# Kernel tuning notes

Measured on AMD Instinct MI355X. Metric: run time of the kernel, lower is better.

Reference implementation:

```python
import jax, jax.numpy as jnp
import numpy as np

EPS = 1e-5  # torch BatchNorm1d default eps


def _bn(x, axes):
    # BatchNorm in training mode with gamma=1, beta=0 (torch init values):
    # normalize with biased batch statistics over the given axes.
    m = x.mean(axes, keepdims=True)
    v = x.var(axes, keepdims=True)
    return (x - m) * jax.lax.rsqrt(v + EPS)


def setup_inputs() -> dict:
    key = jax.random.key(0)
    ks = jax.random.split(key, 12)
    N, M = 50000, 12
    OF, F, E, H = 92, 64, 41, 128
    Z = 2 * F + E  # 169 = concat(node, nbr_node, edge)

    def w(k, shape, fan):
        return jax.random.normal(k, shape, jnp.float32) * np.float32(1.0 / np.sqrt(fan))

    return {
        "node_fea": jax.random.normal(ks[0], (N, OF), jnp.float32),
        "edge_fea": jax.random.uniform(ks[1], (N, M, E), dtype=jnp.float32),
        "nbr_offset": jax.random.randint(ks[2], (N, M, 3), -1, 2).astype(jnp.float32),
        "atom_pos": jax.random.uniform(ks[3], (N, 3), dtype=jnp.float32) * 10.0,
        "cells": jnp.broadcast_to(jnp.eye(3, dtype=jnp.float32) * 10.0, (N, 3, 3))
                 + jax.random.normal(ks[4], (N, 3, 3), jnp.float32) * 0.1,
        "edge_idx": jax.random.randint(ks[5], (N, M), 0, N),
        "W_emb": w(ks[6], (OF, F), OF), "b_emb": jnp.zeros((F,), jnp.float32),
        "W_pre_node": w(ks[7], (3, Z, 2 * F), Z), "b_pre_node": jnp.zeros((3, 2 * F), jnp.float32),
        "W_pre_edge": w(ks[8], (3, Z, 2 * E), Z), "b_pre_edge": jnp.zeros((3, 2 * E), jnp.float32),
        "W_dist": w(ks[9], (Z, H), Z), "b_dist": jnp.zeros((H,), jnp.float32),
        "W_const": w(ks[10], (Z, H), Z), "b_const": jnp.zeros((H,), jnp.float32),
    }


def reference(node_fea, edge_fea, nbr_offset, atom_pos, cells, edge_idx,
              W_emb, b_emb, W_pre_node, b_pre_node, W_pre_edge, b_pre_edge,
              W_dist, b_dist, W_const, b_const):
    N, M = edge_idx.shape
    lrelu = jax.nn.leaky_relu  # torch LeakyReLU default slope 0.01
    sig = jax.nn.sigmoid
    sp = jax.nn.softplus

    # get_distance: neighbor Cartesian positions via unit-cell offsets
    off_cart = jnp.einsum('nmi,nij->nmj', nbr_offset, cells)         # (N,M,3)
    diff = atom_pos[edge_idx] + off_cart - atom_pos[:, None, :]       # (N,M,3)
    distance = jnp.sqrt(jnp.sum(diff * diff, -1, keepdims=True) + 1e-12)  # (N,M,1)

    node = node_fea @ W_emb + b_emb  # embedding -> (N,64)

    for l in range(W_pre_node.shape[0]):  # n_conv = 3 ConvLayers
        nbr = node[edge_idx]  # gather (N,M,F)
        z = jnp.concatenate(
            [jnp.broadcast_to(node[:, None, :], (N, M, node.shape[-1])), nbr, edge_fea],
            axis=2)  # (N,M,169)
        # node branch: linear -> BN -> sigmoid*leakyrelu gate -> sum over M -> BN -> residual
        zn = _bn(z @ W_pre_node[l] + b_pre_node[l], (0, 1))  # (N,M,128)
        nf, nc = jnp.split(zn, 2, axis=2)
        aggr = jnp.sum(sig(nf) * lrelu(nc), axis=1)           # (N,64)
        node = lrelu(node + _bn(aggr, (0,)))
        # edge branch: linear -> BN -> gate -> BN -> residual
        ze = _bn(z @ W_pre_edge[l] + b_pre_edge[l], (0, 1))   # (N,M,82)
        ef, ec = jnp.split(ze, 2, axis=2)
        edge_fea = lrelu(edge_fea + _bn(sig(ef) * lrelu(ec), (0, 1)))

    nbr = node[edge_idx]
    bond_fea = jnp.concatenate(
        [jnp.broadcast_to(node[:, None, :], (N, M, node.shape[-1])), nbr, edge_fea],
        axis=2)  # (N,M,169)

    # n_h_dist == 1 branch: softplus(BN(linear) + distance), mean over channels
    bd = sp(_bn(bond_fea @ W_dist + b_dist, (0, 1)) + distance)
    bd = jnp.mean(bd, axis=2, keepdims=True)                  # (N,M,1)
    # n_h_const == 1 branch: softplus(BN(linear)), mean over channels, / N
    bc = sp(_bn(bond_fea @ W_const + b_const, (0, 1)))
    bc = jnp.mean(bc, axis=2, keepdims=True) / N              # (N,M,1)

    return jnp.concatenate([bd, bc], axis=2)                  # (N,M,2)
```

## Files before the change

kernel.cpp:

```cpp
#include <hip/hip_runtime.h>
#include <math.h>

#define NN 50000
#define MM 12
#define NM 600000
#define OF 92
#define FF 64
#define EE 41
#define ES 48
#define ZZ 169
#define EFO 128
#define ECO 192
#define RPB 96
#define NPB 8
#define NBLK 6250
#define KP 200
#define KSTEPS 6
#define MT 6
#define NSLICE 64
#define PSTRIDE 1024

typedef __bf16 bf16x8 __attribute__((ext_vector_type(8)));
typedef float  f32x4  __attribute__((ext_vector_type(4)));

__device__ __forceinline__ float lrelu(float x){ return fmaxf(x, 0.01f*x); }
__device__ __forceinline__ float sigm(float x){ return __builtin_amdgcn_rcpf(1.f+__expf(-x)); }
__device__ __forceinline__ float softpl(float x){ return fmaxf(x,0.f) + __logf(1.f+__expf(-fabsf(x))); }
__device__ __forceinline__ unsigned short f2bf(float f){
    __bf16 h = (__bf16)f;
    return __builtin_bit_cast(unsigned short, h);
}
__device__ __forceinline__ float b2f(unsigned short u){
    unsigned int b = ((unsigned int)u) << 16;
    return __builtin_bit_cast(float, b);
}
__device__ __forceinline__ unsigned short f2h(float f){
    _Float16 h = (_Float16)f;
    return __builtin_bit_cast(unsigned short, h);
}
__device__ __forceinline__ float h2f(unsigned short u){
    return (float)__builtin_bit_cast(_Float16, u);
}

__global__ __launch_bounds__(256) void pack_w(const float* __restrict__ Wn,
    const float* __restrict__ We, const float* __restrict__ Wd,
    const float* __restrict__ Wc, unsigned short* __restrict__ dst)
{
    int idx = blockIdx.x*256 + threadIdx.x;
    if (idx >= 4*49152) return;
    int j    = idx & 7;
    int lane = (idx >> 3) & 63;
    int ntks = (idx >> 9) % 96;
    int L    = idx / 49152;
    int nt = ntks & 15, ks = ntks >> 4;
    int k   = ks*32 + (lane>>4)*8 + j;
    int col = nt*16 + (lane&15);
    float v = 0.f;
    if (k < ZZ) {
        if (L < 3) {
            if (col < 128)                       v = Wn[((size_t)L*ZZ + k)*128 + col];
            else if (col >= EFO && col < EFO+EE) v = We[((size_t)L*ZZ + k)*82 + (col-EFO)];
            else if (col >= ECO && col < ECO+EE) v = We[((size_t)L*ZZ + k)*82 + 41 + (col-ECO)];
        } else {
            if (col < 128) v = Wd[(size_t)k*128 + col];
            else           v = Wc[(size_t)k*128 + (col-128)];
        }
    }
    dst[idx] = f2bf(v);
}

__global__ __launch_bounds__(256) void k_dist(const float* __restrict__ off,
    const float* __restrict__ apos, const float* __restrict__ cells,
    const int* __restrict__ eidx, float* __restrict__ distb)
{
    int idx = blockIdx.x*256 + threadIdx.x;
    if (idx >= NM) return;
    int n = idx / MM;
    const float* o  = off + (size_t)idx*3;
    const float* cl = cells + (size_t)n*9;
    int n2 = eidx[idx];
    float o0=o[0], o1=o[1], o2=o[2];
    float dd = 1e-12f;
    #pragma unroll
    for (int j=0;j<3;j++){
        float oc = o0*cl[0*3+j] + o1*cl[1*3+j] + o2*cl[2*3+j];
        float d = apos[(size_t)n2*3+j] + oc - apos[(size_t)n*3+j];
        dd += d*d;
    }
    distb[idx] = sqrtf(dd);
}

__global__ __launch_bounds__(256) void k_cvt(const float* __restrict__ src,
    unsigned short* __restrict__ e)
{
    int idx = blockIdx.x*256 + threadIdx.x;
    if (idx >= NM*ES) return;
    int gr = idx / ES;
    int c  = idx - gr*ES;
    e[idx] = (c < EE) ? f2bf(src[(size_t)gr*EE + c]) : (unsigned short)0;
}

__global__ __launch_bounds__(256) void k_emb(const float* __restrict__ nf,
    const float* __restrict__ W, const float* __restrict__ b,
    unsigned short* __restrict__ node0)
{
    int idx = blockIdx.x*256 + threadIdx.x;
    if (idx >= NN*FF) return;
    int n = idx >> 6, c = idx & 63;
    float s = b[c];
    for (int k=0;k<OF;k++) s = fmaf(nf[(size_t)n*OF+k], W[k*FF+c], s);
    node0[idx] = f2bf(s);
}

__global__ __launch_bounds__(256) void k_red(float* __restrict__ P,
    float* __restrict__ dst, int lo, int hi)
{
    for (int c = lo + threadIdx.x; c < hi; c += 256) {
        float s = 0.f;
        #pragma unroll 8
        for (int sl = 0; sl < NSLICE; ++sl) s += P[sl*PSTRIDE + c];
        dst[c] = s;
        #pragma unroll 8
        for (int sl = 0; sl < NSLICE; ++sl) P[sl*PSTRIDE + c] = 0.f;
    }
}

__device__ __forceinline__ void stage_z(unsigned short* __restrict__ Zl,
    const unsigned short* __restrict__ node_src, const unsigned short* __restrict__ edge_src,
    const int* __restrict__ eidx, int n0, int tid)
{
    const int gr0 = n0 * MM;
    #pragma unroll
    for (int it=0; it<3; ++it){
        int i = it*256 + tid;
        int row = i >> 3, ch = i & 7;
        int n = n0 + row/MM;
        uint4 v = *(const uint4*)(node_src + (size_t)n*FF + ch*8);
        *(uint4*)(Zl + row*KP + ch*8) = v;
    }
    #pragma unroll
    for (int it=0; it<3; ++it){
        int i = it*256 + tid;
        int row = i >> 3, ch = i & 7;
        int n2 = eidx[gr0 + row];
        uint4 v = *(const uint4*)(node_src + (size_t)n2*FF + ch*8);
        *(uint4*)(Zl + row*KP + 64 + ch*8) = v;
    }
    #pragma unroll
    for (int it=0; it<3; ++it){
        int i = it*256 + tid;
        int row = i >> 3, ch = i & 7;
        uint4 v = make_uint4(0u,0u,0u,0u);
        if (ch < 6) v = *(const uint4*)(edge_src + (size_t)(gr0+row)*ES + ch*8);
        *(uint4*)(Zl + row*KP + 128 + ch*8) = v;
    }
}

__device__ __forceinline__ void mfma_core(const unsigned short* __restrict__ Zl,
    const unsigned short* __restrict__ Wpk, int w, int lane, f32x4 (&acc)[MT][4])
{
    const int quad = lane >> 4, li = lane & 15;
    #pragma unroll
    for (int mt=0;mt<MT;mt++)
        #pragma unroll
        for (int t=0;t<4;t++) acc[mt][t] = (f32x4){0.f,0.f,0.f,0.f};

    #pragma unroll 2
    for (int ks=0; ks<KSTEPS; ++ks) {
        bf16x8 bfr[4];
        #pragma unroll
        for (int t=0;t<4;t++){
            int nt = w + 4*t;
            bfr[t] = *(const bf16x8*)(Wpk + (((ks*16 + nt)*64 + lane) << 3));
        }
        bf16x8 afr[MT];
        #pragma unroll
        for (int mt=0;mt<MT;mt++){
            int row = mt*16 + li;
            afr[mt] = *(const bf16x8*)(Zl + row*KP + ks*32 + quad*8);
        }
        #pragma unroll
        for (int mt=0;mt<MT;mt++)
            #pragma unroll
            for (int t=0;t<4;t++)
                acc[mt][t] = __builtin_amdgcn_mfma_f32_16x16x32_bf16(afr[mt], bfr[t], acc[mt][t], 0, 0, 0);
    }
}

__device__ __forceinline__ void stats_epi(const f32x4 (&acc)[MT][4], int w, int lane,
    float* __restrict__ Ps)
{
    const int quad = lane>>4, li = lane&15;
    #pragma unroll
    for (int t=0;t<4;t++){
        float s=0.f, q=0.f;
        #pragma unroll
        for (int mt=0;mt<MT;mt++)
            #pragma unroll
            for (int r=0;r<4;r++){ float v = acc[mt][t][r]; s+=v; q = fmaf(v,v,q); }
        s += __shfl_xor(s,16); s += __shfl_xor(s,32);
        q += __shfl_xor(q,16); q += __shfl_xor(q,32);
        if (quad == 0) {
            int col = t*64 + w*16 + li;
            atomicAdd(&Ps[col], s);
            atomicAdd(&Ps[256+col], q);
        }
    }
}

__global__ __launch_bounds__(256) void k_stats(
    const unsigned short* __restrict__ node_src, const unsigned short* __restrict__ edge_src,
    const int* __restrict__ eidx, const unsigned short* __restrict__ Wpk,
    float* __restrict__ Pst)
{
    __shared__ unsigned short Zl[RPB*KP];
    const int tid = threadIdx.x, w = tid>>6, lane = tid&63;
    const int n0 = blockIdx.x * NPB;
    stage_z(Zl, node_src, edge_src, eidx, n0, tid);
    __syncthreads();
    f32x4 acc[MT][4];
    mfma_core(Zl, Wpk, w, lane, acc);
    float* Ps = Pst + (size_t)(blockIdx.x & (NSLICE-1))*PSTRIDE;
    stats_epi(acc, w, lane, Ps);
}

__global__ __launch_bounds__(256) void k_gemm(
    const unsigned short* __restrict__ node_src, const unsigned short* __restrict__ edge_src,
    const int* __restrict__ eidx, const unsigned short* __restrict__ Wpk,
    float* __restrict__ Pst, ushort4* __restrict__ Y)
{
    __shared__ unsigned short Zl[RPB*KP];
    const int tid = threadIdx.x, w = tid>>6, lane = tid&63;
    const int b = blockIdx.x;
    const int n0 = b * NPB;
    stage_z(Zl, node_src, edge_src, eidx, n0, tid);
    __syncthreads();
    f32x4 acc[MT][4];
    mfma_core(Zl, Wpk, w, lane, acc);
    #pragma unroll
    for (int mt=0;mt<MT;mt++)
        #pragma unroll
        for (int t=0;t<4;t++){
            ushort4 h;
            h.x = f2h(acc[mt][t][0]); h.y = f2h(acc[mt][t][1]);
            h.z = f2h(acc[mt][t][2]); h.w = f2h(acc[mt][t][3]);
            Y[((size_t)b*96 + mt*16 + t*4 + w)*64 + lane] = h;
        }
    float* Ps = Pst + (size_t)(blockIdx.x & (NSLICE-1))*PSTRIDE;
    stats_epi(acc, w, lane, Ps);
}

__device__ __forceinline__ void apply_epi(float (&vals)[4], int mt,
    int quad, int cg, bool ce_ok, const float sc[4], const float bi[4],
    int r, int gr0, float* __restrict__ gL, unsigned short* __restrict__ gbuf,
    float& pg, float& pq)
{
    int row = mt*16 + quad*4 + r;
    float nf = fmaf(vals[0], sc[0], bi[0]);
    float nc = fmaf(vals[1], sc[1], bi[1]);
    gL[row*68 + cg] = sigm(nf) * lrelu(nc);
    if (ce_ok) {
        float ef = fmaf(vals[2], sc[2], bi[2]);
        float ec = fmaf(vals[3], sc[3], bi[3]);
        float gv = sigm(ef)*lrelu(ec);
        gbuf[(size_t)(gr0+row)*ES + cg] = f2bf(gv);
        pg += gv; pq = fmaf(gv,gv,pq);
    }
}

__device__ __forceinline__ void apply_tail(float pg, float pq, int tid, int quad,
    int cg, bool ce_ok, int n0, const float* __restrict__ gL,
    float* __restrict__ aggr, float* __restrict__ aS, float* __restrict__ aQ,
    float* __restrict__ gS, float* __restrict__ gQ)
{
    pg += __shfl_xor(pg,16); pg += __shfl_xor(pg,32);
    pq += __shfl_xor(pq,16); pq += __shfl_xor(pq,32);
    if (quad==0 && ce_ok){ atomicAdd(&gS[cg], pg); atomicAdd(&gQ[cg], pq); }
    __syncthreads();
    if (tid < 64) {
        float sAcc=0.f, sQq=0.f;
        #pragma unroll
        for (int nl=0; nl<NPB; nl++){
            float vsum = 0.f;
            #pragma unroll
            for (int jj=0;jj<MM;jj++) vsum += gL[(nl*MM+jj)*68 + tid];
            aggr[(size_t)(n0+nl)*64 + tid] = vsum;
            sAcc += vsum; sQq = fmaf(vsum,vsum,sQq);
        }
        atomicAdd(&aS[tid], sAcc);
        atomicAdd(&aQ[tid], sQq);
    }
}

__global__ __launch_bounds__(256) void k_apply_y(
    const ushort4* __restrict__ Y,
    const float* __restrict__ preS, const float* __restrict__ preQ,
    float* __restrict__ aggr, unsigned short* __restrict__ gbuf,
    float* __restrict__ Pst)
{
    __shared__ float gL[RPB*68];
    const int tid = threadIdx.x, w = tid>>6, lane = tid&63;
    const int quad = lane>>4, li = lane&15;
    const int b = blockIdx.x;
    const int n0 = b * NPB;
    const int gr0 = n0 * MM;
    const int cg = w*16 + li;

    float sc[4], bi[4];
    #pragma unroll
    for (int t=0;t<4;t++){
        int col = t*64 + cg;
        float mm = preS[col]*(1.f/(float)NM);
        float vv = preQ[col]*(1.f/(float)NM) - mm*mm;
        float is = rsqrtf(vv + 1e-5f);
        sc[t] = is; bi[t] = -mm*is;
    }

    float pg = 0.f, pq = 0.f;
    const bool ce_ok = cg < EE;
    #pragma unroll
    for (int mt=0;mt<MT;mt++){
        unsigned short a[4][4];
        #pragma unroll
        for (int t=0;t<4;t++)
            *(ushort4*)a[t] = Y[((size_t)b*96 + mt*16 + t*4 + w)*64 + lane];
        #pragma unroll
        for (int r=0;r<4;r++){
            float vals[4] = {h2f(a[0][r]), h2f(a[1][r]), h2f(a[2][r]), h2f(a[3][r])};
            apply_epi(vals, mt, quad, cg, ce_ok, sc, bi, r, gr0, gL, gbuf, pg, pq);
        }
    }
    float* Ps = Pst + (size_t)(b & (NSLICE-1))*PSTRIDE;
    apply_tail(pg, pq, tid, quad, cg, ce_ok, n0, gL, aggr, Ps+512, Ps+576, Ps+640, Ps+704);
}

__global__ __launch_bounds__(256) void k_apply_re(
    const unsigned short* __restrict__ node_src, const unsigned short* __restrict__ edge_src,
    const int* __restrict__ eidx, const unsigned short* __restrict__ Wpk,
    const float* __restrict__ preS, const float* __restrict__ preQ,
    float* __restrict__ aggr, unsigned short* __restrict__ gbuf,
    float* __restrict__ Pst)
{
    __shared__ __align__(16) char smem[RPB*KP*2];
    unsigned short* Zl = (unsigned short*)smem;
    float* gL = (float*)smem;
    const int tid = threadIdx.x, w = tid>>6, lane = tid&63;
    const int quad = lane>>4, li = lane&15;
    const int n0 = blockIdx.x * NPB;
    const int gr0 = n0 * MM;
    stage_z(Zl, node_src, edge_src, eidx, n0, tid);
    __syncthreads();
    f32x4 acc[MT][4];
    mfma_core(Zl, Wpk, w, lane, acc);
    __syncthreads();

    const int cg = w*16 + li;
    float sc[4], bi[4];
    #pragma unroll
    for (int t=0;t<4;t++){
        int col = t*64 + cg;
        float mm = preS[col]*(1.f/(float)NM);
        float vv = preQ[col]*(1.f/(float)NM) - mm*mm;
        float is = rsqrtf(vv + 1e-5f);
        sc[t] = is; bi[t] = -mm*is;
    }
    float pg = 0.f, pq = 0.f;
    const bool ce_ok = cg < EE;
    #pragma unroll
    for (int mt=0;mt<MT;mt++)
        #pragma unroll
        for (int r=0;r<4;r++){
            float vals[4] = {acc[mt][0][r], acc[mt][1][r], acc[mt][2][r], acc[mt][3][r]};
            apply_epi(vals, mt, quad, cg, ce_ok, sc, bi, r, gr0, gL, gbuf, pg, pq);
        }
    float* Ps = Pst + (size_t)(blockIdx.x & (NSLICE-1))*PSTRIDE;
    apply_tail(pg, pq, tid, quad, cg, ce_ok, n0, gL, aggr, Ps+512, Ps+576, Ps+640, Ps+704);
}

__global__ __launch_bounds__(256) void k_upd_node(const unsigned short* __restrict__ cur,
    const float* __restrict__ aggr, const float* __restrict__ aS,
    const float* __restrict__ aQ, unsigned short* __restrict__ nxt)
{
    int idx = blockIdx.x*256 + threadIdx.x;
    if (idx >= NN*8) return;
    int n = idx >> 3, ch = idx & 7;
    int base = n*64 + ch*8;
    float4 a0 = *(const float4*)(aggr + base);
    float4 a1 = *(const float4*)(aggr + base + 4);
    uint4 cu = *(const uint4*)(cur + base);
    unsigned short cs[8]; *(uint4*)cs = cu;
    float av[8] = {a0.x,a0.y,a0.z,a0.w,a1.x,a1.y,a1.z,a1.w};
    unsigned short os[8];
    #pragma unroll
    for (int j=0;j<8;j++){
        int c = ch*8+j;
        float mm = aS[c]*(1.f/(float)NN);
        float vv = aQ[c]*(1.f/(float)NN) - mm*mm;
        float is = rsqrtf(vv + 1e-5f);
        float v = (av[j] - mm) * is;
        os[j] = f2bf(lrelu(b2f(cs[j]) + v));
    }
    *(uint4*)(nxt + base) = *(uint4*)os;
}

__global__ __launch_bounds__(256) void k_upd_edge(unsigned short* __restrict__ e,
    const unsigned short* __restrict__ g, const float* __restrict__ gS,
    const float* __restrict__ gQ)
{
    int idx = blockIdx.x*256 + threadIdx.x;
    if (idx >= NM*6) return;
    int gr = idx / 6, ch = idx - gr*6;
    size_t base = (size_t)gr*ES + ch*8;
    uint4 eu = *(const uint4*)(e + base);
    uint4 gu = *(const uint4*)(g + base);
    unsigned short es8[8], gs8[8], os[8];
    *(uint4*)es8 = eu; *(uint4*)gs8 = gu;
    #pragma unroll
    for (int j=0;j<8;j++){
        int c = ch*8+j;
        if (c < EE) {
            float mm = gS[c]*(1.f/(float)NM);
            float vv = gQ[c]*(1.f/(float)NM) - mm*mm;
            float is = rsqrtf(vv + 1e-5f);
            float v = (b2f(gs8[j]) - mm) * is;
            os[j] = f2bf(lrelu(b2f(es8[j]) + v));
        } else {
            os[j] = es8[j];
        }
    }
    *(uint4*)(e + base) = *(uint4*)os;
}

__device__ __forceinline__ void final_epi(const float vals[4], int mt, int r,
    int quad, int w, int liq, bool wr, const float sc[4], const float bi[4],
    int gr0, const float* __restrict__ distb,
    float* __restrict__ bufD, float* __restrict__ bufC)
{
    int row = mt*16 + quad*4 + r;
    float dv = distb[gr0 + row];
    float pd = softpl(fmaf(vals[0],sc[0],bi[0]) + dv)
             + softpl(fmaf(vals[1],sc[1],bi[1]) + dv);
    float pc = softpl(fmaf(vals[2],sc[2],bi[2]))
             + softpl(fmaf(vals[3],sc[3],bi[3]));
    pd += __shfl_xor(pd,1); pd += __shfl_xor(pd,2);
    pc += __shfl_xor(pc,1); pc += __shfl_xor(pc,2);
    if (wr) {
        bufD[row*17 + w*4 + liq] = pd;
        bufC[row*17 + w*4 + liq] = pc;
    }
}

__device__ __forceinline__ void final_tail(int tid, int gr0,
    const float* __restrict__ bufD, const float* __restrict__ bufC,
    float* __restrict__ out)
{
    __syncthreads();
    if (tid < 2*RPB) {
        int h = tid >= RPB;
        int row = tid - (h ? RPB : 0);
        const float* buf = h ? bufC : bufD;
        float s = 0.f;
        #pragma unroll
        for (int t=0;t<16;t++) s += buf[row*17+t];
        size_t gr = gr0 + row;
        out[gr*2 + h] = h ? s * (1.f/128.f) * (1.f/(float)NN) : s * (1.f/128.f);
    }
}

__global__ __launch_bounds__(256) void k_final_y(
    const ushort4* __restrict__ Y,
    const float* __restrict__ fS, const float* __restrict__ fQ,
    const float* __restrict__ distb, float* __restrict__ out)
{
    __shared__ float bufD[RPB*17];
    __shared__ float bufC[RPB*17];
    const int tid = threadIdx.x, w = tid>>6, lane = tid&63;
    const int quad = lane>>4, li = lane&15;
    const int b = blockIdx.x;
    const int gr0 = b * NPB * MM;
    const int cg = w*16 + li;

    float sc[4], bi[4];
    #pragma unroll
    for (int t=0;t<4;t++){
        int col = t*64 + cg;
        float mm = fS[col]*(1.f/(float)NM);
        float vv = fQ[col]*(1.f/(float)NM) - mm*mm;
        float is = rsqrtf(vv + 1e-5f);
        sc[t] = is; bi[t] = -mm*is;
    }
    const int liq = li >> 2;
    const bool wr = (li & 3) == 0;
    #pragma unroll
    for (int mt=0;mt<MT;mt++){
        unsigned short a[4][4];
        #pragma unroll
        for (int t=0;t<4;t++)
            *(ushort4*)a[t] = Y[((size_t)b*96 + mt*16 + t*4 + w)*64 + lane];
        #pragma unroll
        for (int r=0;r<4;r++){
            float vals[4] = {h2f(a[0][r]), h2f(a[1][r]), h2f(a[2][r]), h2f(a[3][r])};
            final_epi(vals, mt, r, quad, w, liq, wr, sc, bi, gr0, distb, bufD, bufC);
        }
    }
    final_tail(tid, gr0, bufD, bufC, out);
}

__global__ __launch_bounds__(256) void k_final_re(
    const unsigned short* __restrict__ node_src, const unsigned short* __restrict__ edge_src,
    const int* __restrict__ eidx, const unsigned short* __restrict__ Wpk,
    const float* __restrict__ fS, const float* __restrict__ fQ,
    const float* __restrict__ distb, float* __restrict__ out)
{
    __shared__ __align__(16) char smem[RPB*KP*2];
    unsigned short* Zl = (unsigned short*)smem;
    float* bufD = (float*)smem;
    float* bufC = (float*)(smem + 8192);
    const int tid = threadIdx.x, w = tid>>6, lane = tid&63;
    const int quad = lane>>4, li = lane&15;
    const int n0 = blockIdx.x * NPB;
    const int gr0 = n0 * MM;
    stage_z(Zl, node_src, edge_src, eidx, n0, tid);
    __syncthreads();
    f32x4 acc[MT][4];
    mfma_core(Zl, Wpk, w, lane, acc);
    __syncthreads();

    const int cg = w*16 + li;
    float sc[4], bi[4];
    #pragma unroll
    for (int t=0;t<4;t++){
        int col = t*64 + cg;
        float mm = fS[col]*(1.f/(float)NM);
        float vv = fQ[col]*(1.f/(float)NM) - mm*mm;
        float is = rsqrtf(vv + 1e-5f);
        sc[t] = is; bi[t] = -mm*is;
    }
    const int liq = li >> 2;
    const bool wr = (li & 3) == 0;
    #pragma unroll
    for (int mt=0;mt<MT;mt++)
        #pragma unroll
        for (int r=0;r<4;r++){
            float vals[4] = {acc[mt][0][r], acc[mt][1][r], acc[mt][2][r], acc[mt][3][r]};
            final_epi(vals, mt, r, quad, w, liq, wr, sc, bi, gr0, distb, bufD, bufC);
        }
    final_tail(tid, gr0, bufD, bufC, out);
}

extern "C" void kernel_launch(void* const* d_in, const int* in_sizes, int n_in,
                              void* d_out, int out_size, void* d_ws, size_t ws_size,
                              hipStream_t stream)
{
    const float* node_fea = (const float*)d_in[0];
    const float* edge_in  = (const float*)d_in[1];
    const float* nbr_off  = (const float*)d_in[2];
    const float* apos     = (const float*)d_in[3];
    const float* cells    = (const float*)d_in[4];
    const int*   eidx     = (const int*)  d_in[5];
    const float* W_emb    = (const float*)d_in[6];
    const float* b_emb    = (const float*)d_in[7];
    const float* W_pn     = (const float*)d_in[8];
    const float* W_pe     = (const float*)d_in[10];
    const float* W_dist   = (const float*)d_in[12];
    const float* W_cst    = (const float*)d_in[14];
    float* out = (float*)d_out;
    char* ws = (char*)d_ws;

    size_t o = 0;
    auto alloc = [&](size_t bytes) { char* p = ws + o; o += (bytes + 255) & ~(size_t)255; return p; };
    unsigned short* node0 = (unsigned short*)alloc((size_t)NN*FF*2);
    unsigned short* node1 = (unsigned short*)alloc((size_t)NN*FF*2);
    unsigned short* ebuf  = (unsigned short*)alloc((size_t)NM*ES*2);
    unsigned short* gbuf  = (unsigned short*)alloc((size_t)NM*ES*2);
    float* aggr  = (float*)alloc((size_t)NN*FF*4);
    float* distb = (float*)alloc((size_t)NM*4);
    unsigned short* Wpk = (unsigned short*)alloc((size_t)4*49152*2);
    float* stats = (float*)alloc(4096*4);
    float* Pst   = (float*)alloc((size_t)NSLICE*PSTRIDE*4);

    const size_t YB = (size_t)NBLK*96*64*8;
    const bool useY = (o + YB) <= ws_size;
    ushort4* Ybuf = useY ? (ushort4*)alloc(YB) : (ushort4*)nullptr;

    hipMemsetAsync(stats, 0, 4096*sizeof(float), stream);
    hipMemsetAsync(Pst, 0, (size_t)NSLICE*PSTRIDE*sizeof(float), stream);
    pack_w<<<(4*49152+255)/256, 256, 0, stream>>>(W_pn, W_pe, W_dist, W_cst, Wpk);
    k_dist <<<(NM+255)/256,     256, 0, stream>>>(nbr_off, apos, cells, eidx, distb);
    k_cvt  <<<(NM*ES+255)/256,  256, 0, stream>>>(edge_in, ebuf);
    k_emb  <<<(NN*FF+255)/256,  256, 0, stream>>>(node_fea, W_emb, b_emb, node0);

    const unsigned short* ncur = node0;

    for (int l=0;l<3;l++){
        float* st = stats + l*768;
        float* preS = st;       float* preQ = st+256;
        float* aSs  = st+512;   float* aQq  = st+576;
        float* gSs  = st+640;   float* gQq  = st+704;
        const unsigned short* Wl = Wpk + (size_t)l*49152;
        unsigned short* ndst = (l & 1) ? node0 : node1;

        if (useY) {
            k_gemm   <<<NBLK,256,0,stream>>>(ncur, ebuf, eidx, Wl, Pst, Ybuf);
            k_red    <<<1,256,0,stream>>>(Pst, st, 0, 512);
            k_apply_y<<<NBLK,256,0,stream>>>(Ybuf, preS, preQ, aggr, gbuf, Pst);
            k_red    <<<1,256,0,stream>>>(Pst, st, 512, 768);
        } else {
            k_stats  <<<NBLK,256,0,stream>>>(ncur, ebuf, eidx, Wl, Pst);
            k_red    <<<1,256,0,stream>>>(Pst, st, 0, 512);
            k_apply_re<<<NBLK,256,0,stream>>>(ncur, ebuf, eidx, Wl, preS, preQ,
                                              aggr, gbuf, Pst);
            k_red    <<<1,256,0,stream>>>(Pst, st, 512, 768);
        }
        k_upd_node<<<(NN*8+255)/256,256,0,stream>>>(ncur, aggr, aSs, aQq, ndst);
        k_upd_edge<<<(NM*6+255)/256,256,0,stream>>>(ebuf, gbuf, gSs, gQq);
        ncur = ndst;
    }

    float* fSt = stats + 3*768;
    float* fS = fSt; float* fQ = fSt + 256;
    const unsigned short* Wf = Wpk + (size_t)3*49152;
    if (useY) {
        k_gemm   <<<NBLK,256,0,stream>>>(ncur, ebuf, eidx, Wf, Pst, Ybuf);
        k_red    <<<1,256,0,stream>>>(Pst, fSt, 0, 512);
        k_final_y<<<NBLK,256,0,stream>>>(Ybuf, fS, fQ, distb, out);
    } else {
        k_stats  <<<NBLK,256,0,stream>>>(ncur, ebuf, eidx, Wf, Pst);
        k_red    <<<1,256,0,stream>>>(Pst, fSt, 0, 512);
        k_final_re<<<NBLK,256,0,stream>>>(ncur, ebuf, eidx, Wf, fS, fQ, distb, out);
    }
}
```

Measured before the change: 1.358 ms.

## Compute pre-activation BN statistics from the Gram matrix of Z

Adds a path, used when the Y buffer does not fit in the workspace, that builds the 176x176 Gram matrix Z^T Z per layer with bf16 MFMA over the upper-triangular 16x16 tile pairs. Per-channel sums and sums of squares of Z·W then come from w^T S w and the bias-column row of S, in place of a full stats GEMM pass. This removes the redundant GEMM and projection work of the stats pass, but adds partial-sum buffers, atomics and an extra reduction. Taking variance as E[x²]−mean² from bf16 inputs may lose precision.

```diff
diff --git a/kernel.cpp b/kernel.cpp
--- a/kernel.cpp
+++ b/kernel.cpp
@@ -20,6 +20,14 @@
 #define NSLICE 64
 #define PSTRIDE 1024
 
+#define ZTP 104
+#define NPR 66
+
+#define ZTZ_PI {0,0,0,0,0,0,0,0,0,0,0, 1,1,1,1,1,1,1,1,1,1, 2,2,2,2,2,2,2,2,2, \
+                3,3,3,3,3,3,3,3, 4,4,4,4,4,4,4, 5,5,5,5,5,5, 6,6,6,6,6, 7,7,7,7, 8,8,8, 9,9, 10}
+#define ZTZ_PJ {0,1,2,3,4,5,6,7,8,9,10, 1,2,3,4,5,6,7,8,9,10, 2,3,4,5,6,7,8,9,10, \
+                3,4,5,6,7,8,9,10, 4,5,6,7,8,9,10, 5,6,7,8,9,10, 6,7,8,9,10, 7,8,9,10, 8,9,10, 9,10, 10}
+
 typedef __bf16 bf16x8 __attribute__((ext_vector_type(8)));
 typedef float  f32x4  __attribute__((ext_vector_type(4)));
 
@@ -125,6 +133,154 @@
     }
 }
 
+__device__ __forceinline__ void stage_zt(unsigned short* __restrict__ Zt,
+    const unsigned short* __restrict__ node_src, const unsigned short* __restrict__ edge_src,
+    const int* __restrict__ eidx, int n0, int tid)
+{
+    const int gr0 = n0 * MM;
+    #pragma unroll
+    for (int it=0; it<3; ++it){
+        int i = it*256 + tid;
+        int r = i >> 3, ch = i & 7;
+        int n = n0 + r/MM;
+        uint4 v = *(const uint4*)(node_src + (size_t)n*FF + ch*8);
+        unsigned short s[8]; *(uint4*)s = v;
+        #pragma unroll
+        for (int j=0;j<8;j++) Zt[(ch*8+j)*ZTP + r] = s[j];
+    }
+    #pragma unroll
+    for (int it=0; it<3; ++it){
+        int i = it*256 + tid;
+        int r = i >> 3, ch = i & 7;
+        int n2 = eidx[gr0 + r];
+        uint4 v = *(const uint4*)(node_src + (size_t)n2*FF + ch*8);
+        unsigned short s[8]; *(uint4*)s = v;
+        #pragma unroll
+        for (int j=0;j<8;j++) Zt[(64+ch*8+j)*ZTP + r] = s[j];
+    }
+    #pragma unroll
+    for (int it=0; it<3; ++it){
+        int i = it*256 + tid;
+        int r = i >> 3, ch = i & 7;
+        if (ch < 6) {
+            uint4 v = *(const uint4*)(edge_src + (size_t)(gr0+r)*ES + ch*8);
+            unsigned short s[8]; *(uint4*)s = v;
+            #pragma unroll
+            for (int j=0;j<8;j++){
+                int c = ch*8 + j;
+                unsigned short val = (c == EE) ? (unsigned short)0x3F80 : s[j];
+                Zt[(128+c)*ZTP + r] = val;
+            }
+        }
+    }
+}
+
+template<int W>
+__device__ __forceinline__ void ztz_mfma(const unsigned short* __restrict__ Zt,
+    int lane, f32x4 (&acc)[17])
+{
+    constexpr int PI[NPR] = ZTZ_PI;
+    constexpr int PJ[NPR] = ZTZ_PJ;
+    const int quad = lane >> 4, li = lane & 15;
+    #pragma unroll
+    for (int ks=0; ks<3; ++ks){
+        bf16x8 fr[11];
+        #pragma unroll
+        for (int t=0;t<11;t++)
+            fr[t] = *(const bf16x8*)(Zt + (t*16+li)*ZTP + ks*32 + quad*8);
+        #pragma unroll
+        for (int p=0;p<17;p++){
+            if (W + 4*p < NPR)
+                acc[p] = __builtin_amdgcn_mfma_f32_16x16x32_bf16(
+                    fr[PI[W+4*p]], fr[PJ[W+4*p]], acc[p], 0, 0, 0);
+        }
+    }
+}
+
+__global__ __launch_bounds__(256) void k_ztz(
+    const unsigned short* __restrict__ node_src, const unsigned short* __restrict__ edge_src,
+    const int* __restrict__ eidx, float* __restrict__ Spart)
+{
+    __shared__ unsigned short Zt[176*ZTP];
+    const int tid = threadIdx.x, w = tid>>6, lane = tid&63;
+    f32x4 acc[17];
+    #pragma unroll
+    for (int p=0;p<17;p++) acc[p] = (f32x4){0.f,0.f,0.f,0.f};
+
+    for (int tb = blockIdx.x; tb < NBLK; tb += gridDim.x){
+        stage_zt(Zt, node_src, edge_src, eidx, tb*NPB, tid);
+        __syncthreads();
+        if      (w==0) ztz_mfma<0>(Zt, lane, acc);
+        else if (w==1) ztz_mfma<1>(Zt, lane, acc);
+        else if (w==2) ztz_mfma<2>(Zt, lane, acc);
+        else           ztz_mfma<3>(Zt, lane, acc);
+        __syncthreads();
+    }
+    float* R = Spart + (size_t)blockIdx.x * (NPR*256);
+    #pragma unroll
+    for (int p=0;p<17;p++){
+        int idx = w + 4*p;
+        if (idx < NPR){
+            #pragma unroll
+            for (int r=0;r<4;r++)
+                R[idx*256 + r*64 + lane] = acc[p][r];
+        }
+    }
+}
+
+__global__ __launch_bounds__(256) void k_sexp(const float* __restrict__ Spart,
+    int nreg, float* __restrict__ S)
+{
+    constexpr int PI[NPR] = ZTZ_PI;
+    constexpr int PJ[NPR] = ZTZ_PJ;
+    const int p = blockIdx.x >> 3, oct = blockIdx.x & 7;
+    const int idx = threadIdx.x;
+    float s = 0.f;
+    for (int b = oct; b < nreg; b += 8)
+        s += Spart[(size_t)b*(NPR*256) + p*256 + idx];
+    int r  = idx >> 6, ln = idx & 63;
+    int row = PI[p]*16 + ((ln>>4)<<2) + r;
+    int col = PJ[p]*16 + (ln&15);
+    atomicAdd(&S[row*176 + col], s);
+    if (PI[p] != PJ[p]) atomicAdd(&S[col*176 + row], s);
+}
+
+__global__ __launch_bounds__(256) void k_bnstat(const float* __restrict__ S,
+    const float* __restrict__ Wa, const float* __restrict__ Wb, int mode,
+    float* __restrict__ outS, float* __restrict__ outQ)
+{
+    __shared__ float wl[176];
+    __shared__ float red[256];
+    const int c = blockIdx.x, tid = threadIdx.x;
+    float wv = 0.f;
+    if (tid < ZZ){
+        float raw = 0.f;
+        if (mode == 0){
+            if (c < 128)                    raw = Wa[tid*128 + c];
+            else if (c < 128+EE)            raw = Wb[tid*82 + (c-128)];
+            else if (c >= ECO && c < ECO+EE) raw = Wb[tid*82 + 41 + (c-ECO)];
+        } else {
+            raw = (c < 128) ? Wa[tid*128 + c] : Wb[tid*128 + (c-128)];
+        }
+        wv = b2f(f2bf(raw));
+    }
+    if (tid < 176) wl[tid] = wv;
+    __syncthreads();
+    float u = 0.f;
+    if (tid < 176){
+        for (int k2=0; k2<ZZ; ++k2)
+            u = fmaf(S[k2*176 + tid], wl[k2], u);
+    }
+    float qp = wv * u;
+    float mp = (tid < ZZ) ? wv * S[tid*176 + 169] : 0.f;
+    red[tid] = qp; __syncthreads();
+    for (int s=128; s>0; s>>=1){ if (tid<s) red[tid] += red[tid+s]; __syncthreads(); }
+    float q = red[0]; __syncthreads();
+    red[tid] = mp; __syncthreads();
+    for (int s=128; s>0; s>>=1){ if (tid<s) red[tid] += red[tid+s]; __syncthreads(); }
+    if (tid == 0){ outS[c] = red[0]; outQ[c] = q; }
+}
+
 __device__ __forceinline__ void stage_z(unsigned short* __restrict__ Zl,
     const unsigned short* __restrict__ node_src, const unsigned short* __restrict__ edge_src,
     const int* __restrict__ eidx, int n0, int tid)
@@ -578,10 +734,19 @@
     unsigned short* Wpk = (unsigned short*)alloc((size_t)4*49152*2);
     float* stats = (float*)alloc(4096*4);
     float* Pst   = (float*)alloc((size_t)NSLICE*PSTRIDE*4);
+    float* Sful  = (float*)alloc((size_t)176*176*4);
 
     const size_t YB = (size_t)NBLK*96*64*8;
     const bool useY = (o + YB) <= ws_size;
     ushort4* Ybuf = useY ? (ushort4*)alloc(YB) : (ushort4*)nullptr;
+
+    int nbz = 0; float* Spart = nullptr;
+    if (!useY) {
+        const size_t sp512 = (size_t)512*NPR*256*4;
+        const size_t sp256 = (size_t)256*NPR*256*4;
+        if (o + sp512 <= ws_size)      { Spart = (float*)alloc(sp512); nbz = 512; }
+        else if (o + sp256 <= ws_size) { Spart = (float*)alloc(sp256); nbz = 256; }
+    }
 
     hipMemsetAsync(stats, 0, 4096*sizeof(float), stream);
     hipMemsetAsync(Pst, 0, (size_t)NSLICE*PSTRIDE*sizeof(float), stream);
@@ -605,6 +770,15 @@
             k_red    <<<1,256,0,stream>>>(Pst, st, 0, 512);
             k_apply_y<<<NBLK,256,0,stream>>>(Ybuf, preS, preQ, aggr, gbuf, Pst);
             k_red    <<<1,256,0,stream>>>(Pst, st, 512, 768);
+        } else if (nbz) {
+            hipMemsetAsync(Sful, 0, (size_t)176*176*4, stream);
+            k_ztz   <<<nbz,256,0,stream>>>(ncur, ebuf, eidx, Spart);
+            k_sexp  <<<NPR*8,256,0,stream>>>(Spart, nbz, Sful);
+            k_bnstat<<<256,256,0,stream>>>(Sful, W_pn + (size_t)l*ZZ*128,
+                                           W_pe + (size_t)l*ZZ*82, 0, preS, preQ);
+            k_apply_re<<<NBLK,256,0,stream>>>(ncur, ebuf, eidx, Wl, preS, preQ,
+                                              aggr, gbuf, Pst);
+            k_red    <<<1,256,0,stream>>>(Pst, st, 512, 768);
         } else {
             k_stats  <<<NBLK,256,0,stream>>>(ncur, ebuf, eidx, Wl, Pst);
             k_red    <<<1,256,0,stream>>>(Pst, st, 0, 512);
@@ -624,6 +798,12 @@
         k_gemm   <<<NBLK,256,0,stream>>>(ncur, ebuf, eidx, Wf, Pst, Ybuf);
         k_red    <<<1,256,0,stream>>>(Pst, fSt, 0, 512);
         k_final_y<<<NBLK,256,0,stream>>>(Ybuf, fS, fQ, distb, out);
+    } else if (nbz) {
+        hipMemsetAsync(Sful, 0, (size_t)176*176*4, stream);
+        k_ztz   <<<nbz,256,0,stream>>>(ncur, ebuf, eidx, Spart);
+        k_sexp  <<<NPR*8,256,0,stream>>>(Spart, nbz, Sful);
+        k_bnstat<<<256,256,0,stream>>>(Sful, W_dist, W_cst, 1, fS, fQ);
+        k_final_re<<<NBLK,256,0,stream>>>(ncur, ebuf, eidx, Wf, fS, fQ, distb, out);
     } else {
         k_stats  <<<NBLK,256,0,stream>>>(ncur, ebuf, eidx, Wf, Pst);
         k_red    <<<1,256,0,stream>>>(Pst, fSt, 0, 512);
```

Measured after the change: 1.451 ms. 6.9% more time.
